# Kernel tuning notes

Measured on AMD Instinct MI355X. Metric: run time of the kernel, lower is better.

Reference implementation:

```python
import jax, jax.numpy as jnp
import numpy as np

UNITS = 128000
NEGATIVES = 8192
N = 8192
C = 1024


def _log_uniform_expected_count(ids, num_sampled, range_max):
    # log-uniform (Zipfian) sampler: P(c) = (log(c+2)-log(c+1))/log(range_max+1)
    idf = ids.astype(jnp.float32)
    p = (jnp.log(idf + 2.0) - jnp.log(idf + 1.0)) / jnp.log(jnp.float32(range_max + 1.0))
    # unique sampling expected count: E = -expm1(num_sampled * log1p(-p))
    return -jnp.expm1(jnp.float32(num_sampled) * jnp.log1p(-p))


def setup_inputs() -> dict:
    key = jax.random.key(0)
    k1, k2, k3, k4, k5 = jax.random.split(key, 5)
    inputs = jax.random.normal(k1, (N, C), dtype=jnp.float32)
    targets = jax.random.randint(k2, (N,), 0, UNITS, dtype=jnp.int32)
    sampled = jax.random.randint(k3, (NEGATIVES,), 0, UNITS, dtype=jnp.int32)
    kernel = jax.random.normal(k4, (UNITS, C), dtype=jnp.float32) * 0.02
    bias = jax.random.normal(k5, (UNITS,), dtype=jnp.float32) * 0.01
    return {"inputs": inputs, "targets": targets, "sampled": sampled, "kernel": kernel, "bias": bias}


def reference(inputs, targets, sampled, kernel, bias):
    # --- tf.nn.sampled_softmax_loss with log_uniform_candidate_sampler ---
    # gather true class rows: [N, C], [N]
    true_w = kernel[targets]
    true_b = bias[targets]
    # gather sampled class rows: [S, C], [S]
    samp_w = kernel[sampled]
    samp_b = bias[sampled]
    # true logits: [N]
    true_logits = jnp.einsum('nc,nc->n', inputs, true_w) + true_b
    # sampled logits: [N, S]
    samp_logits = jnp.einsum('nc,sc->ns', inputs, samp_w) + samp_b[None, :]
    # remove accidental hits (sampled id == true label)
    acc = sampled[None, :] == targets[:, None]
    samp_logits = jnp.where(acc, samp_logits - 1e9, samp_logits)
    # subtract log expected counts (sampling-probability correction)
    true_logits = true_logits - jnp.log(_log_uniform_expected_count(targets, NEGATIVES, UNITS))
    samp_logits = samp_logits - jnp.log(_log_uniform_expected_count(sampled, NEGATIVES, UNITS))[None, :]
    # softmax CE with the true class at column 0
    out_logits = jnp.concatenate([true_logits[:, None], samp_logits], axis=1)  # [N, 1+S]
    per_example = jax.nn.logsumexp(out_logits, axis=-1) - out_logits[:, 0]
    # loss_reduction='sum_over_batch_size' -> mean
    return jnp.mean(per_example)
```

## Files before the change

### kernel.cpp

```cpp
#include <hip/hip_runtime.h>
#include <cstdint>
#include <cstddef>

#define NUNITS 128000
#define NNEG   8192
#define NROWS  8192
#define NC     1024

typedef unsigned short u16;
typedef float  f32x4  __attribute__((ext_vector_type(4)));
typedef __bf16 bf16x8 __attribute__((ext_vector_type(8)));

__device__ __forceinline__ u16 f2bf(float x) {
    unsigned u = __float_as_uint(x);
    u = (u + 0x7FFFu + ((u >> 16) & 1u)) >> 16;
    return (u16)u;
}

__device__ __forceinline__ float log_expected_count(int id) {
    float idf = (float)id;
    float p = (logf(idf + 2.0f) - logf(idf + 1.0f)) / logf((float)NUNITS + 1.0f);
    float e = -expm1f((float)NNEG * log1pf(-p));
    return logf(e);
}

__global__ void cast_inputs_kernel(const float* __restrict__ in, u16* __restrict__ outp) {
    const int i = blockIdx.x * 256 + threadIdx.x;
    const float4 v = ((const float4*)in)[i];
    ushort4 o;
    o.x = f2bf(v.x); o.y = f2bf(v.y); o.z = f2bf(v.z); o.w = f2bf(v.w);
    ((ushort4*)outp)[i] = o;
}

__global__ void gather_w_kernel(const float* __restrict__ kern, const int* __restrict__ sampled,
                                u16* __restrict__ wout) {
    const int srow = blockIdx.x;
    const int id = sampled[srow];
    const float4* src = (const float4*)(kern + (size_t)id * NC);
    ushort4* dst = (ushort4*)(wout + (size_t)srow * NC);
    const float4 v = src[threadIdx.x];
    ushort4 o;
    o.x = f2bf(v.x); o.y = f2bf(v.y); o.z = f2bf(v.z); o.w = f2bf(v.w);
    dst[threadIdx.x] = o;
}

__global__ void bcorr_kernel(const int* __restrict__ sampled, const float* __restrict__ bias,
                             float* __restrict__ bc) {
    const int i = blockIdx.x * 256 + threadIdx.x;
    const int id = sampled[i];
    bc[i] = bias[id] - log_expected_count(id);
}

__global__ void true_logits_kernel(const float* __restrict__ inputs, const int* __restrict__ targets,
                                   const float* __restrict__ kern, const float* __restrict__ bias,
                                   float* __restrict__ truel) {
    const int wv = threadIdx.x >> 6;
    const int lane = threadIdx.x & 63;
    const int row = blockIdx.x * 4 + wv;
    const int t = targets[row];
    const float4* a = (const float4*)(inputs + (size_t)row * NC);
    const float4* w = (const float4*)(kern + (size_t)t * NC);
    float s = 0.0f;
#pragma unroll
    for (int i = 0; i < 4; ++i) {
        float4 x = a[lane + i * 64];
        float4 y = w[lane + i * 64];
        s += x.x * y.x + x.y * y.y + x.z * y.z + x.w * y.w;
    }
    for (int m = 32; m; m >>= 1) s += __shfl_xor(s, m, 64);
    if (lane == 0) truel[row] = s + bias[t] - log_expected_count(t);
}

__global__ __launch_bounds__(256, 2) void gemm_lse_kernel(
    const u16* __restrict__ Abf, const u16* __restrict__ Wbf,
    const float* __restrict__ bcorr, const int* __restrict__ targets,
    const int* __restrict__ sampled, float* __restrict__ partial) {
    __shared__ u16 lds_A[128 * 32];
    __shared__ u16 lds_W[128 * 32];
    __shared__ int   lds_tgt[128];
    __shared__ int   lds_smp[128];
    __shared__ float lds_bc[128];
    __shared__ float lds_rowsum[128];

    const int tid = threadIdx.x;
    const int wv = tid >> 6;
    const int lane = tid & 63;
    const int bn0 = blockIdx.x * 128;
    const int bm0 = blockIdx.y * 128;
    const int wm = (wv >> 1) * 64;
    const int wn = (wv & 1) * 64;

    if (tid < 128) {
        lds_tgt[tid] = targets[bm0 + tid];
        lds_smp[tid] = sampled[bn0 + tid];
        lds_bc[tid] = bcorr[bn0 + tid];
        lds_rowsum[tid] = 0.0f;
    }

    f32x4 acc[4][4];
    const f32x4 zero4 = {0.0f, 0.0f, 0.0f, 0.0f};
#pragma unroll
    for (int i = 0; i < 4; ++i)
#pragma unroll
        for (int j = 0; j < 4; ++j) acc[i][j] = zero4;

    const int c0 = wv * 2;
    const int rsub = lane >> 2;
    const int cseg = (lane & 3) * 8;
    const int arow = lane & 15;
    const int kq = (lane >> 4) * 8;

    for (int kt = 0; kt < NC / 32; ++kt) {
        const int k0 = kt * 32;
#pragma unroll
        for (int c = 0; c < 2; ++c) {
            const int ch = c0 + c;
            const int rl = ch * 16 + rsub;
            const u16* ga = Abf + (size_t)(bm0 + rl) * NC + k0 + cseg;
            const u16* gw = Wbf + (size_t)(bn0 + rl) * NC + k0 + cseg;
            __builtin_amdgcn_global_load_lds(
                (const __attribute__((address_space(1))) void*)ga,
                (__attribute__((address_space(3))) void*)&lds_A[ch * 512], 16, 0, 0);
            __builtin_amdgcn_global_load_lds(
                (const __attribute__((address_space(1))) void*)gw,
                (__attribute__((address_space(3))) void*)&lds_W[ch * 512], 16, 0, 0);
        }
        __syncthreads();

        bf16x8 af[4], bfv[4];
#pragma unroll
        for (int mt = 0; mt < 4; ++mt)
            af[mt] = *(const bf16x8*)&lds_A[(wm + mt * 16 + arow) * 32 + kq];
#pragma unroll
        for (int nt = 0; nt < 4; ++nt)
            bfv[nt] = *(const bf16x8*)&lds_W[(wn + nt * 16 + arow) * 32 + kq];
#pragma unroll
        for (int mt = 0; mt < 4; ++mt)
#pragma unroll
            for (int nt = 0; nt < 4; ++nt)
                acc[mt][nt] = __builtin_amdgcn_mfma_f32_16x16x32_bf16(
                    af[mt], bfv[nt], acc[mt][nt], 0, 0, 0);
        __syncthreads();
    }

#pragma unroll
    for (int mt = 0; mt < 4; ++mt) {
#pragma unroll
        for (int r = 0; r < 4; ++r) {
            const int row_l = wm + mt * 16 + (lane >> 4) * 4 + r;
            const int tg = lds_tgt[row_l];
            float s = 0.0f;
#pragma unroll
            for (int nt = 0; nt < 4; ++nt) {
                const int col_l = wn + nt * 16 + (lane & 15);
                const float logit = acc[mt][nt][r] + lds_bc[col_l];
                s += (lds_smp[col_l] == tg) ? 0.0f : __expf(logit);
            }
#pragma unroll
            for (int m = 1; m < 16; m <<= 1) s += __shfl_xor(s, m, 64);
            if ((lane & 15) == 0) atomicAdd(&lds_rowsum[row_l], s);
        }
    }
    __syncthreads();
    if (tid < 128) partial[(size_t)(bm0 + tid) * 64 + blockIdx.x] = lds_rowsum[tid];
}

__global__ void row_lse_kernel(const float* __restrict__ partial, const float* __restrict__ truel,
                               float* __restrict__ bsums) {
    const int row = blockIdx.x * 256 + threadIdx.x;
    const float* p = partial + (size_t)row * 64;
    float s = 0.0f;
#pragma unroll
    for (int i = 0; i < 64; ++i) s += p[i];
    const float tl = truel[row];
    float v = logf(s + expf(tl)) - tl;
    for (int m = 32; m; m >>= 1) v += __shfl_xor(v, m, 64);
    __shared__ float red[4];
    if ((threadIdx.x & 63) == 0) red[threadIdx.x >> 6] = v;
    __syncthreads();
    if (threadIdx.x == 0) bsums[blockIdx.x] = red[0] + red[1] + red[2] + red[3];
}

__global__ void finalize_kernel(const float* __restrict__ bsums, float* __restrict__ out) {
    float v = (threadIdx.x < 32) ? bsums[threadIdx.x] : 0.0f;
    for (int m = 32; m; m >>= 1) v += __shfl_xor(v, m, 64);
    if (threadIdx.x == 0) out[0] = v / (float)NROWS;
}

extern "C" void kernel_launch(void* const* d_in, const int* in_sizes, int n_in,
                              void* d_out, int out_size, void* d_ws, size_t ws_size,
                              hipStream_t stream) {
    (void)in_sizes; (void)n_in; (void)out_size; (void)ws_size;
    const float* inputs  = (const float*)d_in[0];
    const int*   targets = (const int*)d_in[1];
    const int*   sampled = (const int*)d_in[2];
    const float* kern    = (const float*)d_in[3];
    const float* bias    = (const float*)d_in[4];
    float* out = (float*)d_out;

    char* ws = (char*)d_ws;
    u16* a_bf = (u16*)ws;
    u16* w_bf = (u16*)(ws + (size_t)16 * 1024 * 1024);
    float* bc    = (float*)(ws + (size_t)32 * 1024 * 1024);
    float* truel = (float*)(ws + (size_t)32 * 1024 * 1024 + 32768);
    float* part  = (float*)(ws + (size_t)32 * 1024 * 1024 + 65536);
    float* bsums = (float*)(ws + (size_t)32 * 1024 * 1024 + 65536 +
                            (size_t)NROWS * 64 * 4);

    cast_inputs_kernel<<<dim3(8192), dim3(256), 0, stream>>>(inputs, a_bf);
    gather_w_kernel<<<dim3(8192), dim3(256), 0, stream>>>(kern, sampled, w_bf);
    bcorr_kernel<<<dim3(32), dim3(256), 0, stream>>>(sampled, bias, bc);
    true_logits_kernel<<<dim3(2048), dim3(256), 0, stream>>>(inputs, targets, kern, bias, truel);
    gemm_lse_kernel<<<dim3(64, 64), dim3(256), 0, stream>>>(a_bf, w_bf, bc, targets, sampled, part);
    row_lse_kernel<<<dim3(32), dim3(256), 0, stream>>>(part, truel, bsums);
    finalize_kernel<<<dim3(1), dim3(64), 0, stream>>>(bsums, out);
}
```

Measured before the change: 769.9 us.

## Switch sampled-logit GEMM to scaled FP8 and fuse prep kernels

Quantizes inputs and gathered sampled weight rows to FP8 with fixed power-of-two scales, and runs the GEMM with fp8 MFMA instead of bf16, rescaling the accumulators in the epilogue. This halves operand bytes and raises matrix throughput. The true-logit dot product is fused into the input cast kernel and the bias correction into the weight gather, cutting launches and reads. The partial-sum layout is transposed for coalesced reduction. FP8 precision with fixed scales risks accuracy loss in the logsumexp.

```diff
diff --git a/kernel.cpp b/kernel.cpp
--- a/kernel.cpp
+++ b/kernel.cpp
@@ -8,14 +8,11 @@
 #define NC     1024
 
 typedef unsigned short u16;
-typedef float  f32x4  __attribute__((ext_vector_type(4)));
-typedef __bf16 bf16x8 __attribute__((ext_vector_type(8)));
+typedef float f32x4 __attribute__((ext_vector_type(4)));
 
-__device__ __forceinline__ u16 f2bf(float x) {
-    unsigned u = __float_as_uint(x);
-    u = (u + 0x7FFFu + ((u >> 16) & 1u)) >> 16;
-    return (u16)u;
-}
+#define SCALE_A 16.0f
+#define SCALE_W 256.0f
+#define INV_SCALE (1.0f / (16.0f * 256.0f))
 
 __device__ __forceinline__ float log_expected_count(int id) {
     float idf = (float)id;
@@ -24,59 +21,49 @@
     return logf(e);
 }
 
-__global__ void cast_inputs_kernel(const float* __restrict__ in, u16* __restrict__ outp) {
-    const int i = blockIdx.x * 256 + threadIdx.x;
-    const float4 v = ((const float4*)in)[i];
-    ushort4 o;
-    o.x = f2bf(v.x); o.y = f2bf(v.y); o.z = f2bf(v.z); o.w = f2bf(v.w);
-    ((ushort4*)outp)[i] = o;
+__device__ __forceinline__ int pack_fp8x4(float x, float y, float z, float w) {
+    int p = __builtin_amdgcn_cvt_pk_fp8_f32(x, y, 0, false);
+    p = __builtin_amdgcn_cvt_pk_fp8_f32(z, w, p, true);
+    return p;
 }
 
-__global__ void gather_w_kernel(const float* __restrict__ kern, const int* __restrict__ sampled,
-                                u16* __restrict__ wout) {
-    const int srow = blockIdx.x;
-    const int id = sampled[srow];
-    const float4* src = (const float4*)(kern + (size_t)id * NC);
-    ushort4* dst = (ushort4*)(wout + (size_t)srow * NC);
-    const float4 v = src[threadIdx.x];
-    ushort4 o;
-    o.x = f2bf(v.x); o.y = f2bf(v.y); o.z = f2bf(v.z); o.w = f2bf(v.w);
-    dst[threadIdx.x] = o;
+__global__ void prep_a_kernel(const float* __restrict__ inputs, const int* __restrict__ targets,
+                              const float* __restrict__ kern, const float* __restrict__ bias,
+                              unsigned char* __restrict__ a8, float* __restrict__ truel) {
+    const int row = blockIdx.x;
+    const int tid = threadIdx.x;
+    const int t = targets[row];
+    const float4 x = ((const float4*)(inputs + (size_t)row * NC))[tid];
+    const float4 w = ((const float4*)(kern + (size_t)t * NC))[tid];
+    ((int*)(a8 + (size_t)row * NC))[tid] =
+        pack_fp8x4(x.x * SCALE_A, x.y * SCALE_A, x.z * SCALE_A, x.w * SCALE_A);
+    float s = x.x * w.x + x.y * w.y + x.z * w.z + x.w * w.w;
+    for (int m = 32; m; m >>= 1) s += __shfl_xor(s, m, 64);
+    __shared__ float red[4];
+    if ((tid & 63) == 0) red[tid >> 6] = s;
+    __syncthreads();
+    if (tid == 0)
+        truel[row] = red[0] + red[1] + red[2] + red[3] + bias[t] - log_expected_count(t);
 }
 
-__global__ void bcorr_kernel(const int* __restrict__ sampled, const float* __restrict__ bias,
-                             float* __restrict__ bc) {
-    const int i = blockIdx.x * 256 + threadIdx.x;
-    const int id = sampled[i];
-    bc[i] = bias[id] - log_expected_count(id);
-}
-
-__global__ void true_logits_kernel(const float* __restrict__ inputs, const int* __restrict__ targets,
-                                   const float* __restrict__ kern, const float* __restrict__ bias,
-                                   float* __restrict__ truel) {
-    const int wv = threadIdx.x >> 6;
-    const int lane = threadIdx.x & 63;
-    const int row = blockIdx.x * 4 + wv;
-    const int t = targets[row];
-    const float4* a = (const float4*)(inputs + (size_t)row * NC);
-    const float4* w = (const float4*)(kern + (size_t)t * NC);
-    float s = 0.0f;
-#pragma unroll
-    for (int i = 0; i < 4; ++i) {
-        float4 x = a[lane + i * 64];
-        float4 y = w[lane + i * 64];
-        s += x.x * y.x + x.y * y.y + x.z * y.z + x.w * y.w;
-    }
-    for (int m = 32; m; m >>= 1) s += __shfl_xor(s, m, 64);
-    if (lane == 0) truel[row] = s + bias[t] - log_expected_count(t);
+__global__ void prep_w_kernel(const float* __restrict__ kern, const int* __restrict__ sampled,
+                              const float* __restrict__ bias,
+                              unsigned char* __restrict__ w8, float* __restrict__ bc) {
+    const int srow = blockIdx.x;
+    const int tid = threadIdx.x;
+    const int id = sampled[srow];
+    const float4 v = ((const float4*)(kern + (size_t)id * NC))[tid];
+    ((int*)(w8 + (size_t)srow * NC))[tid] =
+        pack_fp8x4(v.x * SCALE_W, v.y * SCALE_W, v.z * SCALE_W, v.w * SCALE_W);
+    if (tid == 0) bc[srow] = bias[id] - log_expected_count(id);
 }
 
 __global__ __launch_bounds__(256, 2) void gemm_lse_kernel(
-    const u16* __restrict__ Abf, const u16* __restrict__ Wbf,
+    const unsigned char* __restrict__ A8, const unsigned char* __restrict__ W8,
     const float* __restrict__ bcorr, const int* __restrict__ targets,
     const int* __restrict__ sampled, float* __restrict__ partial) {
-    __shared__ u16 lds_A[128 * 32];
-    __shared__ u16 lds_W[128 * 32];
+    __shared__ unsigned char lds_A[128 * 32];
+    __shared__ unsigned char lds_W[128 * 32];
     __shared__ int   lds_tgt[128];
     __shared__ int   lds_smp[128];
     __shared__ float lds_bc[128];
@@ -104,41 +91,35 @@
 #pragma unroll
         for (int j = 0; j < 4; ++j) acc[i][j] = zero4;
 
-    const int c0 = wv * 2;
-    const int rsub = lane >> 2;
-    const int cseg = (lane & 3) * 8;
+    const int srow_st = wv * 32 + (lane >> 1);
+    const int cb = (lane & 1) * 16;
     const int arow = lane & 15;
     const int kq = (lane >> 4) * 8;
 
     for (int kt = 0; kt < NC / 32; ++kt) {
         const int k0 = kt * 32;
-#pragma unroll
-        for (int c = 0; c < 2; ++c) {
-            const int ch = c0 + c;
-            const int rl = ch * 16 + rsub;
-            const u16* ga = Abf + (size_t)(bm0 + rl) * NC + k0 + cseg;
-            const u16* gw = Wbf + (size_t)(bn0 + rl) * NC + k0 + cseg;
-            __builtin_amdgcn_global_load_lds(
-                (const __attribute__((address_space(1))) void*)ga,
-                (__attribute__((address_space(3))) void*)&lds_A[ch * 512], 16, 0, 0);
-            __builtin_amdgcn_global_load_lds(
-                (const __attribute__((address_space(1))) void*)gw,
-                (__attribute__((address_space(3))) void*)&lds_W[ch * 512], 16, 0, 0);
-        }
+        const unsigned char* ga = A8 + (size_t)(bm0 + srow_st) * NC + k0 + cb;
+        const unsigned char* gw = W8 + (size_t)(bn0 + srow_st) * NC + k0 + cb;
+        __builtin_amdgcn_global_load_lds(
+            (const __attribute__((address_space(1))) void*)ga,
+            (__attribute__((address_space(3))) void*)&lds_A[wv * 1024], 16, 0, 0);
+        __builtin_amdgcn_global_load_lds(
+            (const __attribute__((address_space(1))) void*)gw,
+            (__attribute__((address_space(3))) void*)&lds_W[wv * 1024], 16, 0, 0);
         __syncthreads();
 
-        bf16x8 af[4], bfv[4];
+        long af[4], bfv[4];
 #pragma unroll
         for (int mt = 0; mt < 4; ++mt)
-            af[mt] = *(const bf16x8*)&lds_A[(wm + mt * 16 + arow) * 32 + kq];
+            af[mt] = *(const long*)&lds_A[(wm + mt * 16 + arow) * 32 + kq];
 #pragma unroll
         for (int nt = 0; nt < 4; ++nt)
-            bfv[nt] = *(const bf16x8*)&lds_W[(wn + nt * 16 + arow) * 32 + kq];
+            bfv[nt] = *(const long*)&lds_W[(wn + nt * 16 + arow) * 32 + kq];
 #pragma unroll
         for (int mt = 0; mt < 4; ++mt)
 #pragma unroll
             for (int nt = 0; nt < 4; ++nt)
-                acc[mt][nt] = __builtin_amdgcn_mfma_f32_16x16x32_bf16(
+                acc[mt][nt] = __builtin_amdgcn_mfma_f32_16x16x32_fp8_fp8(
                     af[mt], bfv[nt], acc[mt][nt], 0, 0, 0);
         __syncthreads();
     }
@@ -153,7 +134,7 @@
 #pragma unroll
             for (int nt = 0; nt < 4; ++nt) {
                 const int col_l = wn + nt * 16 + (lane & 15);
-                const float logit = acc[mt][nt][r] + lds_bc[col_l];
+                const float logit = acc[mt][nt][r] * INV_SCALE + lds_bc[col_l];
                 s += (lds_smp[col_l] == tg) ? 0.0f : __expf(logit);
             }
 #pragma unroll
@@ -162,16 +143,16 @@
         }
     }
     __syncthreads();
-    if (tid < 128) partial[(size_t)(bm0 + tid) * 64 + blockIdx.x] = lds_rowsum[tid];
+    if (tid < 128)
+        partial[(size_t)blockIdx.x * NROWS + bm0 + tid] = lds_rowsum[tid];
 }
 
 __global__ void row_lse_kernel(const float* __restrict__ partial, const float* __restrict__ truel,
                                float* __restrict__ bsums) {
     const int row = blockIdx.x * 256 + threadIdx.x;
-    const float* p = partial + (size_t)row * 64;
     float s = 0.0f;
 #pragma unroll
-    for (int i = 0; i < 64; ++i) s += p[i];
+    for (int c = 0; c < 64; ++c) s += partial[(size_t)c * NROWS + row];
     const float tl = truel[row];
     float v = logf(s + expf(tl)) - tl;
     for (int m = 32; m; m >>= 1) v += __shfl_xor(v, m, 64);
@@ -199,19 +180,17 @@
     float* out = (float*)d_out;
 
     char* ws = (char*)d_ws;
-    u16* a_bf = (u16*)ws;
-    u16* w_bf = (u16*)(ws + (size_t)16 * 1024 * 1024);
-    float* bc    = (float*)(ws + (size_t)32 * 1024 * 1024);
-    float* truel = (float*)(ws + (size_t)32 * 1024 * 1024 + 32768);
-    float* part  = (float*)(ws + (size_t)32 * 1024 * 1024 + 65536);
-    float* bsums = (float*)(ws + (size_t)32 * 1024 * 1024 + 65536 +
-                            (size_t)NROWS * 64 * 4);
+    unsigned char* a8 = (unsigned char*)ws;
+    unsigned char* w8 = (unsigned char*)(ws + (size_t)8  * 1024 * 1024);
+    float* bc    = (float*)(ws + (size_t)16 * 1024 * 1024);
+    float* truel = (float*)(ws + (size_t)16 * 1024 * 1024 + 32768);
+    float* part  = (float*)(ws + (size_t)16 * 1024 * 1024 + 65536);
+    float* bsums = (float*)(ws + (size_t)16 * 1024 * 1024 + 65536 +
+                            (size_t)64 * NROWS * 4);
 
-    cast_inputs_kernel<<<dim3(8192), dim3(256), 0, stream>>>(inputs, a_bf);
-    gather_w_kernel<<<dim3(8192), dim3(256), 0, stream>>>(kern, sampled, w_bf);
-    bcorr_kernel<<<dim3(32), dim3(256), 0, stream>>>(sampled, bias, bc);
-    true_logits_kernel<<<dim3(2048), dim3(256), 0, stream>>>(inputs, targets, kern, bias, truel);
-    gemm_lse_kernel<<<dim3(64, 64), dim3(256), 0, stream>>>(a_bf, w_bf, bc, targets, sampled, part);
+    prep_a_kernel<<<dim3(8192), dim3(256), 0, stream>>>(inputs, targets, kern, bias, a8, truel);
+    prep_w_kernel<<<dim3(8192), dim3(256), 0, stream>>>(kern, sampled, bias, w8, bc);
+    gemm_lse_kernel<<<dim3(64, 64), dim3(256), 0, stream>>>(a8, w8, bc, targets, sampled, part);
     row_lse_kernel<<<dim3(32), dim3(256), 0, stream>>>(part, truel, bsums);
     finalize_kernel<<<dim3(1), dim3(64), 0, stream>>>(bsums, out);
 }
```

After: 782.9 us. No clear change (+1.7%).
